# Performance work log

Hardware: AMD Instinct MI355X
Metric: run time of the kernel (lower is better)

## Reference

```python
import jax, jax.numpy as jnp
import numpy as np

N, F_IN, F_OUT = 8192, 128, 64
ALPHA = 0.2  # leaky_relu negative slope
MASK_VAL = -9e15


def setup_inputs() -> dict:
    key = jax.random.key(0)
    k1, k2, k3, k4 = jax.random.split(key, 4)
    x = jax.random.normal(k1, (N, F_IN), dtype=jnp.float32)
    adj_matrix = jax.random.randint(k2, (N, N), 0, 2, dtype=jnp.int32)
    W = jax.random.normal(k3, (F_IN, F_OUT), dtype=jnp.float32) * 0.1
    a = jax.random.normal(k4, (2 * F_OUT, 1), dtype=jnp.float32) * 0.1
    return {"x": x, "adj_matrix": adj_matrix, "W": W, "a": a}


def reference(x, adj_matrix, W, a):
    # h = X W : [N, F_out]
    h = x @ W
    f = h.shape[1]
    # concat([h_i, h_j]) @ a == h_i @ a1 + h_j @ a2  -> avoid O(N^2 * 2F) concat
    a1 = a[:f, 0]   # [F_out]
    a2 = a[f:, 0]   # [F_out]
    s1 = h @ a1     # [N] contribution of source node i
    s2 = h @ a2     # [N] contribution of target node j
    e = jax.nn.leaky_relu(s1[:, None] + s2[None, :], negative_slope=ALPHA)  # [N, N]
    att = jnp.where(adj_matrix > 0, e, jnp.float32(MASK_VAL))
    att = jax.nn.softmax(att, axis=1)
    # dropout is identity in eval mode (training=False)
    h_prime = att @ h  # [N, F_out]
    return jax.nn.elu(h_prime)
```

## Files before the change

### kernel.cpp

```cpp
#include <hip/hip_runtime.h>
#include <hip/hip_bf16.h>
#include <math.h>

#define NN 8192
#define FI 128
#define FO 64
#define ALPHA 0.2f
#define KCHUNK 2048

typedef __attribute__((ext_vector_type(8))) short bf16x8;
typedef __attribute__((ext_vector_type(4))) float f32x4;
typedef unsigned int uint;
typedef unsigned short ushort;

__device__ __forceinline__ float lk(float e)   { return fmaxf(e, ALPHA * e); }
__device__ __forceinline__ float elu1(float v) { return v > 0.f ? v : expm1f(v); }
__device__ __forceinline__ float bf2f(ushort u) {
    union { uint u; float f; } x; x.u = ((uint)u) << 16; return x.f;
}
__device__ __forceinline__ short f2bf(float f) {
    union { float f; uint u; } x; x.f = f;
    uint r = x.u + 0x7fffu + ((x.u >> 16) & 1u);
    return (short)(r >> 16);
}

__global__ __launch_bounds__(256) void k_prep(
    const float* __restrict__ x, const float* __restrict__ W,
    const float* __restrict__ a,
    __hip_bfloat16* __restrict__ hT, float* __restrict__ s1, float* __restrict__ s2)
{
    __shared__ float Wl[FI * FO];
    __shared__ float xrow[4][FI];
    const int tid = threadIdx.x;
    for (int i = tid * 4; i < FI * FO; i += 1024)
        *(float4*)&Wl[i] = *(const float4*)&W[i];
    const int wave = tid >> 6, lane = tid & 63;
    const int row  = blockIdx.x * 4 + wave;
    *(float2*)&xrow[wave][lane * 2] = *(const float2*)&x[(size_t)row * FI + lane * 2];
    __syncthreads();
    float h = 0.f;
    #pragma unroll 8
    for (int k = 0; k < FI; ++k)
        h = fmaf(xrow[wave][k], Wl[k * FO + lane], h);
    hT[(size_t)lane * NN + row] = __float2bfloat16(h);
    float p1 = h * a[lane], p2 = h * a[FO + lane];
    #pragma unroll
    for (int off = 32; off >= 1; off >>= 1) {
        p1 += __shfl_xor(p1, off, 64);
        p2 += __shfl_xor(p2, off, 64);
    }
    if (lane == 0) { s1[row] = p1; s2[row] = p2; }
}

__global__ __launch_bounds__(256) void k_s2max(
    const float* __restrict__ s2, float* __restrict__ s2max)
{
    __shared__ float red[256];
    float m = -1e30f;
    for (int i = threadIdx.x; i < NN; i += 256) m = fmaxf(m, s2[i]);
    red[threadIdx.x] = m;
    __syncthreads();
    for (int s = 128; s > 0; s >>= 1) {
        if (threadIdx.x < s) red[threadIdx.x] = fmaxf(red[threadIdx.x], red[threadIdx.x + s]);
        __syncthreads();
    }
    if (threadIdx.x == 0) *s2max = red[0];
}

__global__ __launch_bounds__(256) void k_attn(
    const int* __restrict__ adj, const float* __restrict__ s1v,
    const float* __restrict__ s2v, const float* __restrict__ s2maxp,
    const __hip_bfloat16* __restrict__ hT, float* __restrict__ out)
{
    __shared__ float red[3][64][16];
    __shared__ float zp[4][16];
    const int tid  = threadIdx.x;
    const int ks   = tid >> 6;
    const int lane = tid & 63;
    const int r16  = lane & 15;
    const int g    = lane >> 4;
    const int rowbase = blockIdx.x * 16;
    const int row  = rowbase + r16;

    const float s1 = s1v[row];
    const float mv = s1 + s2maxp[0];
    const float m  = fmaxf(mv, ALPHA * mv);

    f32x4 acc0 = {0,0,0,0}, acc1 = {0,0,0,0}, acc2 = {0,0,0,0}, acc3 = {0,0,0,0};
    float z = 0.f;
    const size_t adjrow = (size_t)row * NN;
    const int j0base = ks * KCHUNK;

    for (int k0 = 0; k0 < KCHUNK; k0 += 32) {
        const int j0 = j0base + k0 + g * 8;
        const int4   adja = *(const int4*)(adj + adjrow + j0);
        const int4   adjb = *(const int4*)(adj + adjrow + j0 + 4);
        const float4 s2a  = *(const float4*)(s2v + j0);
        const float4 s2b  = *(const float4*)(s2v + j0 + 4);
        const bf16x8 b0 = *(const bf16x8*)(hT + (size_t)(r16)      * NN + j0);
        const bf16x8 b1 = *(const bf16x8*)(hT + (size_t)(16 + r16) * NN + j0);
        const bf16x8 b2 = *(const bf16x8*)(hT + (size_t)(32 + r16) * NN + j0);
        const bf16x8 b3 = *(const bf16x8*)(hT + (size_t)(48 + r16) * NN + j0);

        const int   av8[8] = {adja.x, adja.y, adja.z, adja.w, adjb.x, adjb.y, adjb.z, adjb.w};
        const float s2e[8] = {s2a.x, s2a.y, s2a.z, s2a.w, s2b.x, s2b.y, s2b.z, s2b.w};
        bf16x8 af;
        #pragma unroll
        for (int e = 0; e < 8; ++e) {
            const float v  = s1 + s2e[e];
            const float w  = __expf(lk(v) - m);
            const float wm = (av8[e] > 0) ? w : 0.f;
            const short wb = f2bf(wm);
            af[e] = wb;
            z += bf2f((ushort)wb);
        }
        acc0 = __builtin_amdgcn_mfma_f32_16x16x32_bf16(af, b0, acc0, 0, 0, 0);
        acc1 = __builtin_amdgcn_mfma_f32_16x16x32_bf16(af, b1, acc1, 0, 0, 0);
        acc2 = __builtin_amdgcn_mfma_f32_16x16x32_bf16(af, b2, acc2, 0, 0, 0);
        acc3 = __builtin_amdgcn_mfma_f32_16x16x32_bf16(af, b3, acc3, 0, 0, 0);
    }

    z += __shfl_xor(z, 16, 64);
    z += __shfl_xor(z, 32, 64);

    if (ks > 0) {
        float* dst = &red[ks - 1][lane][0];
        #pragma unroll
        for (int r = 0; r < 4; ++r) {
            dst[r]      = acc0[r];
            dst[4 + r]  = acc1[r];
            dst[8 + r]  = acc2[r];
            dst[12 + r] = acc3[r];
        }
    }
    if (lane < 16) zp[ks][lane] = z;
    __syncthreads();

    if (ks == 0) {
        #pragma unroll
        for (int w = 0; w < 3; ++w) {
            const float* src = &red[w][lane][0];
            #pragma unroll
            for (int r = 0; r < 4; ++r) {
                acc0[r] += src[r];
                acc1[r] += src[4 + r];
                acc2[r] += src[8 + r];
                acc3[r] += src[12 + r];
            }
        }
        #pragma unroll
        for (int r = 0; r < 4; ++r) {
            const int rr = g * 4 + r;
            float zt = zp[0][rr] + zp[1][rr] + zp[2][rr] + zp[3][rr];
            if (zt == 0.f) zt = 1.f;
            const size_t o = (size_t)(rowbase + rr) * FO + r16;
            out[o]      = elu1(acc0[r] / zt);
            out[o + 16] = elu1(acc1[r] / zt);
            out[o + 32] = elu1(acc2[r] / zt);
            out[o + 48] = elu1(acc3[r] / zt);
        }
    }
}

extern "C" void kernel_launch(void* const* d_in, const int* in_sizes, int n_in,
                              void* d_out, int out_size, void* d_ws, size_t ws_size,
                              hipStream_t stream)
{
    const float* x = nullptr; const int* adj = nullptr;
    const float* W = nullptr; const float* a = nullptr;
    for (int i = 0; i < n_in; ++i) {
        const long long s = in_sizes[i];
        if      (s == (long long)NN * FI) x   = (const float*)d_in[i];
        else if (s == (long long)NN * NN) adj = (const int*)d_in[i];
        else if (s == (long long)FI * FO) W   = (const float*)d_in[i];
        else if (s == (long long)2 * FO)  a   = (const float*)d_in[i];
    }
    if (!x)   x   = (const float*)d_in[0];
    if (!adj) adj = (const int*)d_in[1];
    if (!W)   W   = (const float*)d_in[2];
    if (!a)   a   = (const float*)d_in[3];
    float* out = (float*)d_out;

    char* ws = (char*)d_ws;
    float*          s1    = (float*)(ws);
    float*          s2    = (float*)(ws + 32768);
    float*          s2max = (float*)(ws + 65536);
    __hip_bfloat16* hT    = (__hip_bfloat16*)(ws + 131072);

    k_prep <<<NN / 4, 256, 0, stream>>>(x, W, a, hT, s1, s2);
    k_s2max<<<1, 256, 0, stream>>>(s2, s2max);
    k_attn <<<NN / 16, 256, 0, stream>>>(adj, s1, s2, s2max, hT, out);
}
```

Before: 126.4 us.

## Split attention K dimension across blocks with partial-sum reduction kernel

The attention kernel now splits each 16-row tile's column range across four blocks instead of four waves of one block. Each block writes partial accumulators and softmax denominators to workspace, and a new finalize kernel sums the partials, normalizes and applies ELU. This raises the grid from 512 to 2048 blocks to improve occupancy and memory-level parallelism on the 256-CU device. The cost is an extra launch and extra global traffic for the partials (about 8 MB).

```diff
diff --git a/kernel.cpp b/kernel.cpp
--- a/kernel.cpp
+++ b/kernel.cpp
@@ -6,7 +6,9 @@
 #define FI 128
 #define FO 64
 #define ALPHA 0.2f
-#define KCHUNK 2048
+#define KSPLIT 4
+#define KSTRIP (NN / KSPLIT)
+#define WSTRIP (KSTRIP / 4)
 
 typedef __attribute__((ext_vector_type(8))) short bf16x8;
 typedef __attribute__((ext_vector_type(4))) float f32x4;
@@ -70,16 +72,19 @@
 __global__ __launch_bounds__(256) void k_attn(
     const int* __restrict__ adj, const float* __restrict__ s1v,
     const float* __restrict__ s2v, const float* __restrict__ s2maxp,
-    const __hip_bfloat16* __restrict__ hT, float* __restrict__ out)
+    const __hip_bfloat16* __restrict__ hT,
+    float* __restrict__ pacc, float* __restrict__ pz)
 {
     __shared__ float red[3][64][16];
     __shared__ float zp[4][16];
     const int tid  = threadIdx.x;
-    const int ks   = tid >> 6;
+    const int wv   = tid >> 6;
     const int lane = tid & 63;
     const int r16  = lane & 15;
     const int g    = lane >> 4;
-    const int rowbase = blockIdx.x * 16;
+    const int mb   = blockIdx.x >> 2;
+    const int ks   = blockIdx.x & 3;
+    const int rowbase = mb * 16;
     const int row  = rowbase + r16;
 
     const float s1 = s1v[row];
@@ -89,9 +94,9 @@
     f32x4 acc0 = {0,0,0,0}, acc1 = {0,0,0,0}, acc2 = {0,0,0,0}, acc3 = {0,0,0,0};
     float z = 0.f;
     const size_t adjrow = (size_t)row * NN;
-    const int j0base = ks * KCHUNK;
-
-    for (int k0 = 0; k0 < KCHUNK; k0 += 32) {
+    const int j0base = ks * KSTRIP + wv * WSTRIP;
+
+    for (int k0 = 0; k0 < WSTRIP; k0 += 32) {
         const int j0 = j0base + k0 + g * 8;
         const int4   adja = *(const int4*)(adj + adjrow + j0);
         const int4   adjb = *(const int4*)(adj + adjrow + j0 + 4);
@@ -123,8 +128,8 @@
     z += __shfl_xor(z, 16, 64);
     z += __shfl_xor(z, 32, 64);
 
-    if (ks > 0) {
-        float* dst = &red[ks - 1][lane][0];
+    if (wv > 0) {
+        float* dst = &red[wv - 1][lane][0];
         #pragma unroll
         for (int r = 0; r < 4; ++r) {
             dst[r]      = acc0[r];
@@ -133,10 +138,10 @@
             dst[12 + r] = acc3[r];
         }
     }
-    if (lane < 16) zp[ks][lane] = z;
+    if (lane < 16) zp[wv][lane] = z;
     __syncthreads();
 
-    if (ks == 0) {
+    if (wv == 0) {
         #pragma unroll
         for (int w = 0; w < 3; ++w) {
             const float* src = &red[w][lane][0];
@@ -148,18 +153,35 @@
                 acc3[r] += src[12 + r];
             }
         }
+        float* paccb = pacc + (size_t)ks * NN * FO;
         #pragma unroll
         for (int r = 0; r < 4; ++r) {
             const int rr = g * 4 + r;
-            float zt = zp[0][rr] + zp[1][rr] + zp[2][rr] + zp[3][rr];
-            if (zt == 0.f) zt = 1.f;
             const size_t o = (size_t)(rowbase + rr) * FO + r16;
-            out[o]      = elu1(acc0[r] / zt);
-            out[o + 16] = elu1(acc1[r] / zt);
-            out[o + 32] = elu1(acc2[r] / zt);
-            out[o + 48] = elu1(acc3[r] / zt);
-        }
-    }
+            paccb[o]      = acc0[r];
+            paccb[o + 16] = acc1[r];
+            paccb[o + 32] = acc2[r];
+            paccb[o + 48] = acc3[r];
+        }
+        if (lane < 16)
+            pz[ks * NN + rowbase + lane] = zp[0][lane] + zp[1][lane] + zp[2][lane] + zp[3][lane];
+    }
+}
+
+__global__ __launch_bounds__(256) void k_final(
+    const float* __restrict__ pacc, const float* __restrict__ pz,
+    float* __restrict__ out)
+{
+    const int idx  = blockIdx.x * 256 + threadIdx.x;
+    const int rowi = idx >> 6;
+    float s = 0.f, zt = 0.f;
+    #pragma unroll
+    for (int ks = 0; ks < KSPLIT; ++ks) {
+        s  += pacc[(size_t)ks * NN * FO + idx];
+        zt += pz[ks * NN + rowi];
+    }
+    if (zt == 0.f) zt = 1.f;
+    out[idx] = elu1(s / zt);
 }
 
 extern "C" void kernel_launch(void* const* d_in, const int* in_sizes, int n_in,
@@ -186,8 +208,11 @@
     float*          s2    = (float*)(ws + 32768);
     float*          s2max = (float*)(ws + 65536);
     __hip_bfloat16* hT    = (__hip_bfloat16*)(ws + 131072);
+    float*          pz    = (float*)(ws + 1179648);
+    float*          pacc  = (float*)(ws + 1310720);
 
     k_prep <<<NN / 4, 256, 0, stream>>>(x, W, a, hT, s1, s2);
     k_s2max<<<1, 256, 0, stream>>>(s2, s2max);
-    k_attn <<<NN / 16, 256, 0, stream>>>(adj, s1, s2, s2max, hT, out);
-}
+    k_attn <<<(NN / 16) * KSPLIT, 256, 0, stream>>>(adj, s1, s2, s2max, hT, pacc, pz);
+    k_final<<<(NN * FO) / 256, 256, 0, stream>>>(pacc, pz, out);
+}
```

Measured after the change: 133.6 us. +5.6%, slower.
